# Kernel tuning notes

Hardware: AMD Instinct MI355X
Metric: run time of the kernel (lower is better)

## Reference

```python
import jax, jax.numpy as jnp
import numpy as np

B, N, C, H, NH, NC = 4, 2048, 256, 128, 8, 3  # batch, points, in_ch, hidden, heads, classes
DH = H // NH


def setup_inputs() -> dict:
    key = jax.random.key(0)
    ki = iter(jax.random.split(key, 48))
    def w(shape, s=0.05):
        return jax.random.normal(next(ki), shape, jnp.float32) * s
    z = lambda n: jnp.zeros((n,), jnp.float32)
    o = lambda n: jnp.ones((n,), jnp.float32)
    inp = dict(x=jax.random.normal(next(ki), (B, N, C), jnp.float32))
    inp.update(fuse_w1=w((H, C)), fuse_b1=z(H), fuse_w2=w((H, H)), fuse_b2=z(H))
    for l in range(2):
        inp[f'attn{l}_in_w'] = w((3 * H, H)); inp[f'attn{l}_in_b'] = z(3 * H)
        inp[f'attn{l}_out_w'] = w((H, H)); inp[f'attn{l}_out_b'] = z(H)
        inp[f'ffn{l}_w1'] = w((2 * H, H)); inp[f'ffn{l}_b1'] = z(2 * H)
        inp[f'ffn{l}_w2'] = w((H, 2 * H)); inp[f'ffn{l}_b2'] = z(H)
        inp[f'ln{2*l}_g'] = o(H); inp[f'ln{2*l}_b'] = z(H)
        inp[f'ln{2*l+1}_g'] = o(H); inp[f'ln{2*l+1}_b'] = z(H)
    inp.update(out_w1=w((H, H)), out_b1=z(H), out_w2=w((NC, H)), out_b2=z(NC))
    inp.update(det_w1=w((H // 2, H)), det_b1=z(H // 2), det_w2=w((1, H // 2)), det_b2=z(1))
    return inp


def _ln(x, g, b):
    m = jnp.mean(x, axis=-1, keepdims=True)
    v = jnp.mean((x - m) ** 2, axis=-1, keepdims=True)
    return (x - m) * jax.lax.rsqrt(v + 1e-5) * g + b


def _mha(x, in_w, in_b, out_w, out_b):
    # nn.MultiheadAttention (batch_first, self-attn), eval mode (no dropout)
    Bq, Nq, _ = x.shape
    qkv = x @ in_w.T + in_b                          # [B,N,3H]
    q, k, v = jnp.split(qkv, 3, axis=-1)
    q = q.reshape(Bq, Nq, NH, DH)
    k = k.reshape(Bq, Nq, NH, DH)
    v = v.reshape(Bq, Nq, NH, DH)
    s = jnp.einsum('bqhd,bkhd->bhqk', q, k) / jnp.sqrt(jnp.float32(DH))
    a = jax.nn.softmax(s, axis=-1)
    o = jnp.einsum('bhqk,bkhd->bqhd', a, v).reshape(Bq, Nq, H)
    return o @ out_w.T + out_b


def _forward(x, fuse_w1, fuse_b1, fuse_w2, fuse_b2,
             attn0_in_w, attn0_in_b, attn0_out_w, attn0_out_b,
             ffn0_w1, ffn0_b1, ffn0_w2, ffn0_b2, ln0_g, ln0_b, ln1_g, ln1_b,
             attn1_in_w, attn1_in_b, attn1_out_w, attn1_out_b,
             ffn1_w1, ffn1_b1, ffn1_w2, ffn1_b2, ln2_g, ln2_b, ln3_g, ln3_b,
             out_w1, out_b1, out_w2, out_b2, det_w1, det_b1, det_w2, det_b2):
    # feature_fusion (dropout = identity in eval)
    h = jnp.maximum(x @ fuse_w1.T + fuse_b1, 0) @ fuse_w2.T + fuse_b2
    layers = [
        (attn0_in_w, attn0_in_b, attn0_out_w, attn0_out_b, ffn0_w1, ffn0_b1, ffn0_w2, ffn0_b2, ln0_g, ln0_b, ln1_g, ln1_b),
        (attn1_in_w, attn1_in_b, attn1_out_w, attn1_out_b, ffn1_w1, ffn1_b1, ffn1_w2, ffn1_b2, ln2_g, ln2_b, ln3_g, ln3_b),
    ]
    for (iw, ib, ow, ob, f1w, f1b, f2w, f2b, g1, be1, g2, be2) in layers:
        h = _ln(h + _mha(h, iw, ib, ow, ob), g1, be1)
        h = _ln(h + (jnp.maximum(h @ f1w.T + f1b, 0) @ f2w.T + f2b), g2, be2)
    refined_logits = jnp.maximum(h @ out_w1.T + out_b1, 0) @ out_w2.T + out_b2   # [B,N,NC]
    head_prob = jax.nn.sigmoid(jnp.maximum(h @ det_w1.T + det_b1, 0) @ det_w2.T + det_b2)[..., 0]  # [B,N]
    quality = jnp.mean(head_prob, axis=1)                                        # [B]
    return refined_logits, head_prob, quality


def reference(x, fuse_w1, fuse_b1, fuse_w2, fuse_b2,
              attn0_in_w, attn0_in_b, attn0_out_w, attn0_out_b,
              ffn0_w1, ffn0_b1, ffn0_w2, ffn0_b2, ln0_g, ln0_b, ln1_g, ln1_b,
              attn1_in_w, attn1_in_b, attn1_out_w, attn1_out_b,
              ffn1_w1, ffn1_b1, ffn1_w2, ffn1_b2, ln2_g, ln2_b, ln3_g, ln3_b,
              out_w1, out_b1, out_w2, out_b2, det_w1, det_b1, det_w2, det_b2):
    return _forward(x, fuse_w1, fuse_b1, fuse_w2, fuse_b2,
                    attn0_in_w, attn0_in_b, attn0_out_w, attn0_out_b,
                    ffn0_w1, ffn0_b1, ffn0_w2, ffn0_b2, ln0_g, ln0_b, ln1_g, ln1_b,
                    attn1_in_w, attn1_in_b, attn1_out_w, attn1_out_b,
                    ffn1_w1, ffn1_b1, ffn1_w2, ffn1_b2, ln2_g, ln2_b, ln3_g, ln3_b,
                    out_w1, out_b1, out_w2, out_b2, det_w1, det_b1, det_w2, det_b2)
```

## Files before the change

kernel.cpp:

```cpp
#include <hip/hip_runtime.h>
#include <cstddef>

constexpr int Bb  = 4;
constexpr int Nn  = 2048;
constexpr int Cc  = 256;
constexpr int Hh  = 128;
constexpr int NHh = 8;
constexpr int DHh = 16;
constexpr int MTOK = Bb * Nn;
#define LOG2E 1.4426950408889634f

typedef __attribute__((ext_vector_type(8))) short bf16x8;
typedef __attribute__((ext_vector_type(4))) short bf16x4;
typedef __attribute__((ext_vector_type(4))) float f32x4;

__device__ __forceinline__ short f32_to_bf16_rne(float f) {
    union { float f; unsigned int u; } c; c.f = f;
    unsigned int r = c.u + 0x7fffu + ((c.u >> 16) & 1u);
    return (short)(r >> 16);
}
__device__ __forceinline__ float bf16_to_f32(short s) {
    union { float f; unsigned int u; } c; c.u = ((unsigned int)(unsigned short)s) << 16;
    return c.f;
}
__device__ __forceinline__ unsigned pack2_bf16(float a, float b) {
    unsigned r;
    asm("v_cvt_pk_bf16_f32 %0, %1, %2" : "=v"(r) : "v"(a), "v"(b));
    return r;
}

struct CvtJobs {
    const float* src[13];
    short*       dst[13];
    int          off[14];
    float*       qzero;
};

__global__ __launch_bounds__(256) void cvt_kernel(CvtJobs j) {
    const int gid = blockIdx.x * 256 + threadIdx.x;
    if (blockIdx.x == 0 && threadIdx.x < 4) j.qzero[threadIdx.x] = 0.f;
    if (gid >= j.off[13]) return;
    int k = 0;
    #pragma unroll
    for (int i = 0; i < 12; ++i) if (gid >= j.off[i + 1]) k = i + 1;
    const int idx = (gid - j.off[k]) * 4;
    float4 v = *(const float4*)(j.src[k] + idx);
    short o4[4] = { f32_to_bf16_rne(v.x), f32_to_bf16_rne(v.y),
                    f32_to_bf16_rne(v.z), f32_to_bf16_rne(v.w) };
    *(bf16x4*)(j.dst[k] + idx) = *(bf16x4*)o4;
}

__global__ __launch_bounds__(256) void qkv_gemm_kernel(
    const short* __restrict__ X, const short* __restrict__ W,
    const float* __restrict__ bias, short* __restrict__ Yb)
{
    constexpr int K = 128, N = 384, ST = K + 8;
    __shared__ short As[64 * ST];
    __shared__ short Bs[64 * ST];

    const int tid  = threadIdx.x;
    const int lane = tid & 63;
    const int wv   = tid >> 6;
    const int col  = lane & 15;
    const int g    = lane >> 4;
    const int m0   = blockIdx.y * 64;
    const int n0   = blockIdx.x * 64;

    for (int i = tid; i < 64 * (K / 8); i += 256) {
        const int r = i / (K / 8), c = (i % (K / 8)) * 8;
        *(bf16x8*)&As[r * ST + c] = *(const bf16x8*)(X + (size_t)(m0 + r) * K + c);
        *(bf16x8*)&Bs[r * ST + c] = *(const bf16x8*)(W + (size_t)(n0 + r) * K + c);
    }
    __syncthreads();

    f32x4 acc[4] = {};
    #pragma unroll
    for (int k0 = 0; k0 < K; k0 += 32) {
        bf16x8 a = *(bf16x8*)&As[(wv * 16 + col) * ST + k0 + g * 8];
        #pragma unroll
        for (int jj = 0; jj < 4; ++jj) {
            bf16x8 b = *(bf16x8*)&Bs[(jj * 16 + col) * ST + k0 + g * 8];
            acc[jj] = __builtin_amdgcn_mfma_f32_16x16x32_bf16(a, b, acc[jj], 0, 0, 0);
        }
    }

    #pragma unroll
    for (int jj = 0; jj < 4; ++jj) {
        const int cn = n0 + jj * 16 + col;
        const float bb = bias[cn];
        #pragma unroll
        for (int r = 0; r < 4; ++r) {
            const int rm = m0 + wv * 16 + g * 4 + r;
            Yb[(size_t)rm * N + cn] = f32_to_bf16_rne(acc[jj][r] + bb);
        }
    }
}

template<int K, int CR, bool DO_LN>
__global__ __launch_bounds__(256) void gemmln_kernel(
    const short* __restrict__ X, const short* __restrict__ W,
    const float* __restrict__ bias,
    float* __restrict__ hf, short* __restrict__ hb,
    const float* __restrict__ gw, const float* __restrict__ bw)
{
    constexpr int ST  = K + 8;
    constexpr int NCH = 128 / CR;
    constexpr int NF  = CR / 32;
    __shared__ short As[32 * ST];
    __shared__ short Ws[CR * ST];
    __shared__ float P[32 * 130];

    const int tid  = threadIdx.x;
    const int lane = tid & 63;
    const int wv   = tid >> 6;
    const int col  = lane & 15;
    const int g    = lane >> 4;
    const int m0   = blockIdx.x * 32;
    const int mst  = (wv & 1) * 16;
    const int cb   = (wv >> 1) * (CR / 2);

    for (int i = tid; i < 32 * (K / 8); i += 256) {
        const int r = i / (K / 8), c = (i % (K / 8)) * 8;
        *(bf16x8*)&As[r * ST + c] = *(const bf16x8*)(X + (size_t)(m0 + r) * K + c);
    }

    f32x4 ya[NCH][NF] = {};
    #pragma unroll
    for (int ch = 0; ch < NCH; ++ch) {
        for (int i = tid; i < CR * (K / 8); i += 256) {
            const int r = i / (K / 8), c = (i % (K / 8)) * 8;
            *(bf16x8*)&Ws[r * ST + c] =
                *(const bf16x8*)(W + (size_t)(ch * CR + r) * K + c);
        }
        __syncthreads();
        #pragma unroll
        for (int k0 = 0; k0 < K; k0 += 32) {
            bf16x8 a = *(bf16x8*)&As[(mst + col) * ST + k0 + g * 8];
            #pragma unroll
            for (int f = 0; f < NF; ++f) {
                bf16x8 b = *(bf16x8*)&Ws[(cb + f * 16 + col) * ST + k0 + g * 8];
                ya[ch][f] = __builtin_amdgcn_mfma_f32_16x16x32_bf16(a, b, ya[ch][f], 0, 0, 0);
            }
        }
        __syncthreads();
    }

    #pragma unroll
    for (int ch = 0; ch < NCH; ++ch)
        #pragma unroll
        for (int f = 0; f < NF; ++f) {
            const int cn = ch * CR + cb + f * 16 + col;
            const float bb = bias[cn];
            #pragma unroll
            for (int r = 0; r < 4; ++r)
                P[(mst + g * 4 + r) * 130 + cn] = ya[ch][f][r] + bb;
        }
    __syncthreads();

    #pragma unroll
    for (int rr = 0; rr < 8; ++rr) {
        const int row = wv * 8 + rr;
        const size_t t = m0 + row;
        float2 pv = *(float2*)&P[row * 130 + 2 * lane];
        if (DO_LN) {
            float2 hv = ((const float2*)(hf + t * Hh))[lane];
            float a0 = hv.x + pv.x, a1 = hv.y + pv.y;
            float sum = a0 + a1;
            #pragma unroll
            for (int off = 32; off > 0; off >>= 1) sum += __shfl_xor(sum, off);
            const float mean = sum * (1.f / 128.f);
            const float d0 = a0 - mean, d1 = a1 - mean;
            float vs = d0 * d0 + d1 * d1;
            #pragma unroll
            for (int off = 32; off > 0; off >>= 1) vs += __shfl_xor(vs, off);
            const float rstd = rsqrtf(vs * (1.f / 128.f) + 1e-5f);
            float2 gv = ((const float2*)gw)[lane];
            float2 bv = ((const float2*)bw)[lane];
            float2 r = { d0 * rstd * gv.x + bv.x, d1 * rstd * gv.y + bv.y };
            ((float2*)(hf + t * Hh))[lane] = r;
            *(unsigned*)&hb[t * Hh + lane * 2] = pack2_bf16(r.x, r.y);
        } else {
            ((float2*)(hf + t * Hh))[lane] = pv;
            *(unsigned*)&hb[t * Hh + lane * 2] = pack2_bf16(pv.x, pv.y);
        }
    }
}

template<int K, int MID, int CR1, int CR2, bool DO_LN>
__global__ __launch_bounds__(256) void mlp2_kernel(
    const short* __restrict__ X,
    const short* __restrict__ W1, const float* __restrict__ b1,
    const short* __restrict__ W2, const float* __restrict__ b2,
    float* __restrict__ hf, short* __restrict__ hb,
    const float* __restrict__ gw, const float* __restrict__ bw)
{
    constexpr int STA = K + 8;
    constexpr int STU = MID + 8;
    constexpr int WS1 = CR1 * STA;
    constexpr int WS2 = CR2 * STU;
    constexpr int WSZ = (WS1 > WS2) ? WS1 : WS2;
    __shared__ short As[32 * STA];
    __shared__ short Ws[WSZ];
    __shared__ short U[32 * STU];
    __shared__ float P[32 * 130];

    const int tid  = threadIdx.x;
    const int lane = tid & 63;
    const int wv   = tid >> 6;
    const int col  = lane & 15;
    const int g    = lane >> 4;
    const int m0   = blockIdx.x * 32;
    const int mst  = (wv & 1) * 16;

    for (int i = tid; i < 32 * (K / 8); i += 256) {
        const int r = i / (K / 8), c = (i % (K / 8)) * 8;
        *(bf16x8*)&As[r * STA + c] = *(const bf16x8*)(X + (size_t)(m0 + r) * K + c);
    }

    constexpr int NCH1 = MID / CR1;
    constexpr int NF1  = CR1 / 32;
    const int cb1 = (wv >> 1) * (CR1 / 2);
    #pragma unroll
    for (int ch = 0; ch < NCH1; ++ch) {
        for (int i = tid; i < CR1 * (K / 8); i += 256) {
            const int r = i / (K / 8), c = (i % (K / 8)) * 8;
            *(bf16x8*)&Ws[r * STA + c] =
                *(const bf16x8*)(W1 + (size_t)(ch * CR1 + r) * K + c);
        }
        __syncthreads();
        f32x4 ya[NF1] = {};
        #pragma unroll
        for (int k0 = 0; k0 < K; k0 += 32) {
            bf16x8 a = *(bf16x8*)&As[(mst + col) * STA + k0 + g * 8];
            #pragma unroll
            for (int f = 0; f < NF1; ++f) {
                bf16x8 b = *(bf16x8*)&Ws[(cb1 + f * 16 + col) * STA + k0 + g * 8];
                ya[f] = __builtin_amdgcn_mfma_f32_16x16x32_bf16(a, b, ya[f], 0, 0, 0);
            }
        }
        #pragma unroll
        for (int f = 0; f < NF1; ++f) {
            const int cn = ch * CR1 + cb1 + f * 16 + col;
            const float bb = b1[cn];
            #pragma unroll
            for (int r = 0; r < 4; ++r)
                U[(mst + g * 4 + r) * STU + cn] =
                    f32_to_bf16_rne(fmaxf(ya[f][r] + bb, 0.f));
        }
        __syncthreads();
    }

    constexpr int NCH2 = 128 / CR2;
    constexpr int NF2  = CR2 / 32;
    const int cb2 = (wv >> 1) * (CR2 / 2);
    f32x4 yb[NCH2][NF2] = {};
    #pragma unroll
    for (int ch = 0; ch < NCH2; ++ch) {
        for (int i = tid; i < CR2 * (MID / 8); i += 256) {
            const int r = i / (MID / 8), c = (i % (MID / 8)) * 8;
            *(bf16x8*)&Ws[r * STU + c] =
                *(const bf16x8*)(W2 + (size_t)(ch * CR2 + r) * MID + c);
        }
        __syncthreads();
        #pragma unroll
        for (int k0 = 0; k0 < MID; k0 += 32) {
            bf16x8 a = *(bf16x8*)&U[(mst + col) * STU + k0 + g * 8];
            #pragma unroll
            for (int f = 0; f < NF2; ++f) {
                bf16x8 b = *(bf16x8*)&Ws[(cb2 + f * 16 + col) * STU + k0 + g * 8];
                yb[ch][f] = __builtin_amdgcn_mfma_f32_16x16x32_bf16(a, b, yb[ch][f], 0, 0, 0);
            }
        }
        __syncthreads();
    }

    #pragma unroll
    for (int ch = 0; ch < NCH2; ++ch)
        #pragma unroll
        for (int f = 0; f < NF2; ++f) {
            const int cn = ch * CR2 + cb2 + f * 16 + col;
            const float bb = b2[cn];
            #pragma unroll
            for (int r = 0; r < 4; ++r)
                P[(mst + g * 4 + r) * 130 + cn] = yb[ch][f][r] + bb;
        }
    __syncthreads();

    #pragma unroll
    for (int rr = 0; rr < 8; ++rr) {
        const int row = wv * 8 + rr;
        const size_t t = m0 + row;
        float2 pv = *(float2*)&P[row * 130 + 2 * lane];
        if (DO_LN) {
            float2 hv = ((const float2*)(hf + t * Hh))[lane];
            float a0 = hv.x + pv.x, a1 = hv.y + pv.y;
            float sum = a0 + a1;
            #pragma unroll
            for (int off = 32; off > 0; off >>= 1) sum += __shfl_xor(sum, off);
            const float mean = sum * (1.f / 128.f);
            const float d0 = a0 - mean, d1 = a1 - mean;
            float vs = d0 * d0 + d1 * d1;
            #pragma unroll
            for (int off = 32; off > 0; off >>= 1) vs += __shfl_xor(vs, off);
            const float rstd = rsqrtf(vs * (1.f / 128.f) + 1e-5f);
            float2 gv = ((const float2*)gw)[lane];
            float2 bv = ((const float2*)bw)[lane];
            float2 r = { d0 * rstd * gv.x + bv.x, d1 * rstd * gv.y + bv.y };
            ((float2*)(hf + t * Hh))[lane] = r;
            *(unsigned*)&hb[t * Hh + lane * 2] = pack2_bf16(r.x, r.y);
        } else {
            ((float2*)(hf + t * Hh))[lane] = pv;
            *(unsigned*)&hb[t * Hh + lane * 2] = pack2_bf16(pv.x, pv.y);
        }
    }
}

__global__ __launch_bounds__(256) void head_kernel(
    const short* __restrict__ X,
    const short* __restrict__ W1b, const float* __restrict__ b1,
    const short* __restrict__ DW1b, const float* __restrict__ db1,
    const float* __restrict__ w2, const float* __restrict__ b2,
    const float* __restrict__ dw2, const float* __restrict__ db2,
    float* __restrict__ out)
{
    constexpr int K = 128, ST = K + 8;
    __shared__ short As[32 * ST];
    __shared__ short Ws[64 * ST];
    __shared__ float P[32 * 196];

    const int tid  = threadIdx.x;
    const int lane = tid & 63;
    const int wv   = tid >> 6;
    const int col  = lane & 15;
    const int g    = lane >> 4;
    const int m0   = blockIdx.x * 32;
    const int mst  = (wv & 1) * 16;
    const int cb   = (wv >> 1) * 32;

    for (int i = tid; i < 32 * (K / 8); i += 256) {
        const int r = i / (K / 8), c = (i % (K / 8)) * 8;
        *(bf16x8*)&As[r * ST + c] = *(const bf16x8*)(X + (size_t)(m0 + r) * K + c);
    }

    f32x4 ya[3][2] = {};
    #pragma unroll
    for (int ch = 0; ch < 3; ++ch) {
        for (int i = tid; i < 64 * (K / 8); i += 256) {
            const int r = i / (K / 8), c = (i % (K / 8)) * 8;
            const int rg = ch * 64 + r;
            const short* src = (rg < 128) ? (W1b + (size_t)rg * K)
                                          : (DW1b + (size_t)(rg - 128) * K);
            *(bf16x8*)&Ws[r * ST + c] = *(const bf16x8*)(src + c);
        }
        __syncthreads();
        #pragma unroll
        for (int k0 = 0; k0 < K; k0 += 32) {
            bf16x8 a = *(bf16x8*)&As[(mst + col) * ST + k0 + g * 8];
            #pragma unroll
            for (int f = 0; f < 2; ++f) {
                bf16x8 b = *(bf16x8*)&Ws[(cb + f * 16 + col) * ST + k0 + g * 8];
                ya[ch][f] = __builtin_amdgcn_mfma_f32_16x16x32_bf16(a, b, ya[ch][f], 0, 0, 0);
            }
        }
        __syncthreads();
    }

    #pragma unroll
    for (int ch = 0; ch < 3; ++ch)
        #pragma unroll
        for (int f = 0; f < 2; ++f) {
            const int cn = ch * 64 + cb + f * 16 + col;
            const float bb = (cn < 128) ? b1[cn] : db1[cn - 128];
            #pragma unroll
            for (int r = 0; r < 4; ++r)
                P[(mst + g * 4 + r) * 196 + cn] = fmaxf(ya[ch][f][r] + bb, 0.f);
        }
    __syncthreads();

    const float w20 = w2[2 * lane],       w21 = w2[2 * lane + 1];
    const float w22 = w2[128 + 2 * lane], w23 = w2[129 + 2 * lane];
    const float w24 = w2[256 + 2 * lane], w25 = w2[257 + 2 * lane];
    const float dwl = dw2[lane];
    float qacc = 0.f;
    #pragma unroll
    for (int rr = 0; rr < 8; ++rr) {
        const int row = wv * 8 + rr;
        const size_t t = m0 + row;
        const float x0 = P[row * 196 + 2 * lane];
        const float x1 = P[row * 196 + 2 * lane + 1];
        float s0 = x0 * w20 + x1 * w21;
        float s1 = x0 * w22 + x1 * w23;
        float s2 = x0 * w24 + x1 * w25;
        float d  = P[row * 196 + 128 + lane] * dwl;
        #pragma unroll
        for (int off = 32; off > 0; off >>= 1) {
            s0 += __shfl_xor(s0, off);
            s1 += __shfl_xor(s1, off);
            s2 += __shfl_xor(s2, off);
            d  += __shfl_xor(d,  off);
        }
        if (lane == 0) {
            out[t * 3 + 0] = s0 + b2[0];
            out[t * 3 + 1] = s1 + b2[1];
            out[t * 3 + 2] = s2 + b2[2];
            const float prob = 1.f / (1.f + __expf(-(d + db2[0])));
            out[24576 + t] = prob;
            qacc += prob;
        }
    }
    if (lane == 0)
        atomicAdd(&out[32768 + (m0 >> 11)], qacc * (1.f / (float)Nn));
}

constexpr int KT = 128;
constexpr int KS = 28;
constexpr int VS = 132;

__global__ __launch_bounds__(256) void attn_kernel(
    const short* __restrict__ qkv, short* __restrict__ out)
{
    __shared__ short Ks[KT * KS];
    __shared__ short Vs[DHh * VS];

    const int tid  = threadIdx.x;
    const int lane = tid & 63;
    const int wv   = tid >> 6;
    const int col  = lane & 15;
    const int g    = lane >> 4;
    const int hd   = blockIdx.y;
    const int b    = blockIdx.z;
    const int q0   = blockIdx.x * 64 + wv * 16;

    const short* base = qkv + (size_t)b * Nn * 384;

    bf16x8 qf = {};
    if (g < 2) {
        bf16x8 qraw = *(const bf16x8*)(base + (size_t)(q0 + col) * 384 + hd * DHh + g * 8);
        const float qs = 0.25f * LOG2E;
        #pragma unroll
        for (int i = 0; i < 8; ++i)
            qf[i] = f32_to_bf16_rne(bf16_to_f32(qraw[i]) * qs);
    }

    f32x4 o    = {0.f, 0.f, 0.f, 0.f};
    f32x4 lacc = {0.f, 0.f, 0.f, 0.f};
    const short one_bf16 = (short)0x3F80;
    const bf16x8 ones = { one_bf16, one_bf16, one_bf16, one_bf16,
                          one_bf16, one_bf16, one_bf16, one_bf16 };

    const int ksr = tid >> 1;
    const int ksd = (tid & 1) * 8;
    const int va  = tid >> 2;
    const int vd  = (tid & 3) * 4;

    const short* kptr = base + (size_t)ksr * 384 + Hh + hd * DHh + ksd;
    const short* vptr = base + (size_t)(2 * va) * 384 + 2 * Hh + hd * DHh + vd;
    bf16x8 kreg = *(const bf16x8*)kptr;
    bf16x4 vr0  = *(const bf16x4*)vptr;
    bf16x4 vr1  = *(const bf16x4*)(vptr + 384);

    for (int kt = 0; kt < Nn; kt += KT) {
        __syncthreads();

        *(bf16x8*)&Ks[ksr * KS + ksd] = kreg;
        {
            unsigned a0 = ((const unsigned*)&vr0)[0], a1 = ((const unsigned*)&vr0)[1];
            unsigned b0 = ((const unsigned*)&vr1)[0], b1 = ((const unsigned*)&vr1)[1];
            *(unsigned*)&Vs[(vd + 0) * VS + 2 * va] = __builtin_amdgcn_perm(b0, a0, 0x05040100);
            *(unsigned*)&Vs[(vd + 1) * VS + 2 * va] = __builtin_amdgcn_perm(b0, a0, 0x07060302);
            *(unsigned*)&Vs[(vd + 2) * VS + 2 * va] = __builtin_amdgcn_perm(b1, a1, 0x05040100);
            *(unsigned*)&Vs[(vd + 3) * VS + 2 * va] = __builtin_amdgcn_perm(b1, a1, 0x07060302);
        }

        if (kt + KT < Nn) {
            kptr += KT * 384;
            vptr += KT * 384;
            kreg = *(const bf16x8*)kptr;
            vr0  = *(const bf16x4*)vptr;
            vr1  = *(const bf16x4*)(vptr + 384);
        }

        asm volatile("s_waitcnt lgkmcnt(0)" ::: "memory");
        __builtin_amdgcn_s_barrier();

        __builtin_amdgcn_s_setprio(1);
        #pragma unroll
        for (int s = 0; s < 4; ++s) {
            bf16x8 kf0 = {}, kf1 = {};
            if (g < 2) {
                kf0 = *(bf16x8*)&Ks[(s * 32 + col) * KS + g * 8];
                kf1 = *(bf16x8*)&Ks[(s * 32 + 16 + col) * KS + g * 8];
            }
            f32x4 z = {0.f, 0.f, 0.f, 0.f};
            f32x4 sA = __builtin_amdgcn_mfma_f32_16x16x32_bf16(kf0, qf, z, 0, 0, 0);
            f32x4 sB = __builtin_amdgcn_mfma_f32_16x16x32_bf16(kf1, qf, z, 0, 0, 0);

            union { bf16x8 v; unsigned u[4]; } pf;
            pf.u[0] = pack2_bf16(__builtin_amdgcn_exp2f(sA[0]),
                                 __builtin_amdgcn_exp2f(sA[1]));
            pf.u[1] = pack2_bf16(__builtin_amdgcn_exp2f(sA[2]),
                                 __builtin_amdgcn_exp2f(sA[3]));
            pf.u[2] = pack2_bf16(__builtin_amdgcn_exp2f(sB[0]),
                                 __builtin_amdgcn_exp2f(sB[1]));
            pf.u[3] = pack2_bf16(__builtin_amdgcn_exp2f(sB[2]),
                                 __builtin_amdgcn_exp2f(sB[3]));

            bf16x8 vf;
            ((bf16x4*)&vf)[0] = *(bf16x4*)&Vs[col * VS + s * 32 + g * 4];
            ((bf16x4*)&vf)[1] = *(bf16x4*)&Vs[col * VS + s * 32 + 16 + g * 4];

            o    = __builtin_amdgcn_mfma_f32_16x16x32_bf16(pf.v, vf,   o,    0, 0, 0);
            lacc = __builtin_amdgcn_mfma_f32_16x16x32_bf16(pf.v, ones, lacc, 0, 0, 0);
        }
        __builtin_amdgcn_s_setprio(0);
    }

    #pragma unroll
    for (int r = 0; r < 4; ++r) {
        const float inv = __builtin_amdgcn_rcpf(lacc[r]);
        out[(size_t)(b * Nn + q0 + g * 4 + r) * Hh + hd * DHh + col] =
            f32_to_bf16_rne(o[r] * inv);
    }
}

extern "C" void kernel_launch(void* const* d_in, const int* in_sizes, int n_in,
                              void* d_out, int out_size, void* d_ws, size_t ws_size,
                              hipStream_t stream)
{
    char* W8 = (char*)d_ws;
    float* hf   = (float*)(W8 + 0);
    short* hb   = (short*)(W8 + 4194304);
    short* wb   = (short*)(W8 + 6291456);
    char*  regA = W8 + 7340032;
    char*  regB = W8 + 13631488;

    short* xb    = (short*)regA;
    short* qkvb  = (short*)regA;
    short* attno = (short*)regB;
    float* out   = (float*)d_out;

    const int wsz[12]  = {32768,16384,49152,16384,32768,32768,49152,16384,32768,32768,16384,8192};
    const int wsrc[12] = {1, 3, 5, 7, 9, 11, 17, 19, 21, 23, 29, 33};
    int woff[13]; woff[0] = 0;
    for (int i = 0; i < 12; ++i) woff[i + 1] = woff[i] + wsz[i];

    CvtJobs jobs;
    int acc = 0;
    for (int i = 0; i < 12; ++i) {
        jobs.src[i] = (const float*)d_in[wsrc[i]];
        jobs.dst[i] = wb + woff[i];
        jobs.off[i] = acc;
        acc += wsz[i] / 4;
    }
    jobs.src[12] = (const float*)d_in[0];
    jobs.dst[12] = xb;
    jobs.off[12] = acc;
    acc += (MTOK * Cc) / 4;
    jobs.off[13] = acc;
    jobs.qzero = out + 32768;

    hipLaunchKernelGGL(cvt_kernel, dim3((acc + 255) / 256), dim3(256), 0, stream, jobs);

    hipLaunchKernelGGL((mlp2_kernel<256, 128, 32, 64, false>), dim3(MTOK / 32), dim3(256), 0,
                       stream, xb, wb + woff[0], (const float*)d_in[2],
                       wb + woff[1], (const float*)d_in[4], hf, hb, nullptr, nullptr);

    for (int l = 0; l < 2; ++l) {
        const int ib = 5 + l * 12;
        const int wbase = 2 + l * 4;
        hipLaunchKernelGGL(qkv_gemm_kernel, dim3(384 / 64, MTOK / 64), dim3(256), 0, stream,
                           hb, wb + woff[wbase + 0], (const float*)d_in[ib + 1], qkvb);
        hipLaunchKernelGGL(attn_kernel, dim3(Nn / 64, NHh, Bb), dim3(256), 0, stream,
                           qkvb, attno);
        hipLaunchKernelGGL((gemmln_kernel<128, 64, true>), dim3(MTOK / 32), dim3(256), 0, stream,
                           attno, wb + woff[wbase + 1], (const float*)d_in[ib + 3],
                           hf, hb, (const float*)d_in[ib + 8], (const float*)d_in[ib + 9]);
        hipLaunchKernelGGL((mlp2_kernel<128, 256, 64, 32, true>), dim3(MTOK / 32), dim3(256), 0,
                           stream, hb, wb + woff[wbase + 2], (const float*)d_in[ib + 5],
                           wb + woff[wbase + 3], (const float*)d_in[ib + 7],
                           hf, hb, (const float*)d_in[ib + 10], (const float*)d_in[ib + 11]);
    }

    hipLaunchKernelGGL(head_kernel, dim3(MTOK / 32), dim3(256), 0, stream,
                       hb, wb + woff[10], (const float*)d_in[30],
                       wb + woff[11], (const float*)d_in[34],
                       (const float*)d_in[31], (const float*)d_in[32],
                       (const float*)d_in[35], (const float*)d_in[36], out);
}
```

Baseline: 289.0 us.

## Shrink row tile to 16 tokens and alias LDS epilogue buffer onto weight tile

The fused GEMM+LayerNorm and two-layer MLP kernels now process 16 token rows per block instead of 32, doubling the grid. Each wave owns one 16-column slice per 64-row weight chunk, and K is split into 128-wide stages so the weight tile stays a fixed 64x136. The fp32 epilogue buffer P now reuses the weight-tile shared memory rather than having its own allocation. The aim is lower LDS and register use per block, giving more resident blocks and better latency hiding. The cost is that each weight matrix is reloaded from global/L2 twice as many times in total.

```diff
diff --git a/kernel.cpp b/kernel.cpp
--- a/kernel.cpp
+++ b/kernel.cpp
@@ -96,70 +96,62 @@
     }
 }
 
-template<int K, int CR, bool DO_LN>
+template<int K, bool DO_LN>
 __global__ __launch_bounds__(256) void gemmln_kernel(
     const short* __restrict__ X, const short* __restrict__ W,
     const float* __restrict__ bias,
     float* __restrict__ hf, short* __restrict__ hb,
     const float* __restrict__ gw, const float* __restrict__ bw)
 {
-    constexpr int ST  = K + 8;
-    constexpr int NCH = 128 / CR;
-    constexpr int NF  = CR / 32;
-    __shared__ short As[32 * ST];
-    __shared__ short Ws[CR * ST];
-    __shared__ float P[32 * 130];
+    constexpr int ST = K + 8;
+    __shared__ short As[16 * ST];
+    __shared__ short Ws[64 * 136];
+    float* P = (float*)Ws;
 
     const int tid  = threadIdx.x;
     const int lane = tid & 63;
     const int wv   = tid >> 6;
     const int col  = lane & 15;
     const int g    = lane >> 4;
-    const int m0   = blockIdx.x * 32;
-    const int mst  = (wv & 1) * 16;
-    const int cb   = (wv >> 1) * (CR / 2);
-
-    for (int i = tid; i < 32 * (K / 8); i += 256) {
+    const int m0   = blockIdx.x * 16;
+    const int cb   = wv * 16;
+
+    for (int i = tid; i < 16 * (K / 8); i += 256) {
         const int r = i / (K / 8), c = (i % (K / 8)) * 8;
         *(bf16x8*)&As[r * ST + c] = *(const bf16x8*)(X + (size_t)(m0 + r) * K + c);
     }
 
-    f32x4 ya[NCH][NF] = {};
-    #pragma unroll
-    for (int ch = 0; ch < NCH; ++ch) {
-        for (int i = tid; i < CR * (K / 8); i += 256) {
+    f32x4 ya[2] = {};
+    #pragma unroll
+    for (int ch = 0; ch < 2; ++ch) {
+        for (int i = tid; i < 64 * (K / 8); i += 256) {
             const int r = i / (K / 8), c = (i % (K / 8)) * 8;
-            *(bf16x8*)&Ws[r * ST + c] =
-                *(const bf16x8*)(W + (size_t)(ch * CR + r) * K + c);
+            *(bf16x8*)&Ws[r * 136 + c] =
+                *(const bf16x8*)(W + (size_t)(ch * 64 + r) * K + c);
         }
         __syncthreads();
         #pragma unroll
         for (int k0 = 0; k0 < K; k0 += 32) {
-            bf16x8 a = *(bf16x8*)&As[(mst + col) * ST + k0 + g * 8];
-            #pragma unroll
-            for (int f = 0; f < NF; ++f) {
-                bf16x8 b = *(bf16x8*)&Ws[(cb + f * 16 + col) * ST + k0 + g * 8];
-                ya[ch][f] = __builtin_amdgcn_mfma_f32_16x16x32_bf16(a, b, ya[ch][f], 0, 0, 0);
-            }
+            bf16x8 a = *(bf16x8*)&As[col * ST + k0 + g * 8];
+            bf16x8 b = *(bf16x8*)&Ws[(cb + col) * 136 + k0 + g * 8];
+            ya[ch] = __builtin_amdgcn_mfma_f32_16x16x32_bf16(a, b, ya[ch], 0, 0, 0);
         }
         __syncthreads();
     }
 
     #pragma unroll
-    for (int ch = 0; ch < NCH; ++ch)
-        #pragma unroll
-        for (int f = 0; f < NF; ++f) {
-            const int cn = ch * CR + cb + f * 16 + col;
-            const float bb = bias[cn];
-            #pragma unroll
-            for (int r = 0; r < 4; ++r)
-                P[(mst + g * 4 + r) * 130 + cn] = ya[ch][f][r] + bb;
-        }
+    for (int ch = 0; ch < 2; ++ch) {
+        const int cn = ch * 64 + cb + col;
+        const float bb = bias[cn];
+        #pragma unroll
+        for (int r = 0; r < 4; ++r)
+            P[(g * 4 + r) * 130 + cn] = ya[ch][r] + bb;
+    }
     __syncthreads();
 
     #pragma unroll
-    for (int rr = 0; rr < 8; ++rr) {
-        const int row = wv * 8 + rr;
+    for (int rr = 0; rr < 4; ++rr) {
+        const int row = wv * 4 + rr;
         const size_t t = m0 + row;
         float2 pv = *(float2*)&P[row * 130 + 2 * lane];
         if (DO_LN) {
@@ -186,7 +178,7 @@
     }
 }
 
-template<int K, int MID, int CR1, int CR2, bool DO_LN>
+template<int K, int MID, bool DO_LN>
 __global__ __launch_bounds__(256) void mlp2_kernel(
     const short* __restrict__ X,
     const short* __restrict__ W1, const float* __restrict__ b1,
@@ -196,99 +188,87 @@
 {
     constexpr int STA = K + 8;
     constexpr int STU = MID + 8;
-    constexpr int WS1 = CR1 * STA;
-    constexpr int WS2 = CR2 * STU;
-    constexpr int WSZ = (WS1 > WS2) ? WS1 : WS2;
-    __shared__ short As[32 * STA];
-    __shared__ short Ws[WSZ];
-    __shared__ short U[32 * STU];
-    __shared__ float P[32 * 130];
+    __shared__ short As[16 * STA];
+    __shared__ short Ws[64 * 136];
+    __shared__ short U[16 * STU];
+    float* P = (float*)Ws;
 
     const int tid  = threadIdx.x;
     const int lane = tid & 63;
     const int wv   = tid >> 6;
     const int col  = lane & 15;
     const int g    = lane >> 4;
-    const int m0   = blockIdx.x * 32;
-    const int mst  = (wv & 1) * 16;
-
-    for (int i = tid; i < 32 * (K / 8); i += 256) {
+    const int m0   = blockIdx.x * 16;
+    const int cb   = wv * 16;
+
+    for (int i = tid; i < 16 * (K / 8); i += 256) {
         const int r = i / (K / 8), c = (i % (K / 8)) * 8;
         *(bf16x8*)&As[r * STA + c] = *(const bf16x8*)(X + (size_t)(m0 + r) * K + c);
     }
 
-    constexpr int NCH1 = MID / CR1;
-    constexpr int NF1  = CR1 / 32;
-    const int cb1 = (wv >> 1) * (CR1 / 2);
+    constexpr int KP1  = K / 128;
+    constexpr int NCH1 = MID / 64;
     #pragma unroll
     for (int ch = 0; ch < NCH1; ++ch) {
-        for (int i = tid; i < CR1 * (K / 8); i += 256) {
-            const int r = i / (K / 8), c = (i % (K / 8)) * 8;
-            *(bf16x8*)&Ws[r * STA + c] =
-                *(const bf16x8*)(W1 + (size_t)(ch * CR1 + r) * K + c);
-        }
-        __syncthreads();
-        f32x4 ya[NF1] = {};
-        #pragma unroll
-        for (int k0 = 0; k0 < K; k0 += 32) {
-            bf16x8 a = *(bf16x8*)&As[(mst + col) * STA + k0 + g * 8];
-            #pragma unroll
-            for (int f = 0; f < NF1; ++f) {
-                bf16x8 b = *(bf16x8*)&Ws[(cb1 + f * 16 + col) * STA + k0 + g * 8];
-                ya[f] = __builtin_amdgcn_mfma_f32_16x16x32_bf16(a, b, ya[f], 0, 0, 0);
+        f32x4 ya = {};
+        #pragma unroll
+        for (int kh = 0; kh < KP1; ++kh) {
+            for (int i = tid; i < 64 * 16; i += 256) {
+                const int r = i / 16, c = (i % 16) * 8;
+                *(bf16x8*)&Ws[r * 136 + c] =
+                    *(const bf16x8*)(W1 + (size_t)(ch * 64 + r) * K + kh * 128 + c);
             }
-        }
-        #pragma unroll
-        for (int f = 0; f < NF1; ++f) {
-            const int cn = ch * CR1 + cb1 + f * 16 + col;
-            const float bb = b1[cn];
-            #pragma unroll
-            for (int r = 0; r < 4; ++r)
-                U[(mst + g * 4 + r) * STU + cn] =
-                    f32_to_bf16_rne(fmaxf(ya[f][r] + bb, 0.f));
-        }
-        __syncthreads();
-    }
-
-    constexpr int NCH2 = 128 / CR2;
-    constexpr int NF2  = CR2 / 32;
-    const int cb2 = (wv >> 1) * (CR2 / 2);
-    f32x4 yb[NCH2][NF2] = {};
-    #pragma unroll
-    for (int ch = 0; ch < NCH2; ++ch) {
-        for (int i = tid; i < CR2 * (MID / 8); i += 256) {
-            const int r = i / (MID / 8), c = (i % (MID / 8)) * 8;
-            *(bf16x8*)&Ws[r * STU + c] =
-                *(const bf16x8*)(W2 + (size_t)(ch * CR2 + r) * MID + c);
-        }
-        __syncthreads();
-        #pragma unroll
-        for (int k0 = 0; k0 < MID; k0 += 32) {
-            bf16x8 a = *(bf16x8*)&U[(mst + col) * STU + k0 + g * 8];
-            #pragma unroll
-            for (int f = 0; f < NF2; ++f) {
-                bf16x8 b = *(bf16x8*)&Ws[(cb2 + f * 16 + col) * STU + k0 + g * 8];
-                yb[ch][f] = __builtin_amdgcn_mfma_f32_16x16x32_bf16(a, b, yb[ch][f], 0, 0, 0);
+            __syncthreads();
+            #pragma unroll
+            for (int k0 = 0; k0 < 128; k0 += 32) {
+                bf16x8 a = *(bf16x8*)&As[col * STA + kh * 128 + k0 + g * 8];
+                bf16x8 b = *(bf16x8*)&Ws[(cb + col) * 136 + k0 + g * 8];
+                ya = __builtin_amdgcn_mfma_f32_16x16x32_bf16(a, b, ya, 0, 0, 0);
             }
-        }
-        __syncthreads();
-    }
-
-    #pragma unroll
-    for (int ch = 0; ch < NCH2; ++ch)
-        #pragma unroll
-        for (int f = 0; f < NF2; ++f) {
-            const int cn = ch * CR2 + cb2 + f * 16 + col;
-            const float bb = b2[cn];
-            #pragma unroll
-            for (int r = 0; r < 4; ++r)
-                P[(mst + g * 4 + r) * 130 + cn] = yb[ch][f][r] + bb;
-        }
+            __syncthreads();
+        }
+        const int cn = ch * 64 + cb + col;
+        const float bb = b1[cn];
+        #pragma unroll
+        for (int r = 0; r < 4; ++r)
+            U[(g * 4 + r) * STU + cn] = f32_to_bf16_rne(fmaxf(ya[r] + bb, 0.f));
+    }
+
+    constexpr int KP2 = MID / 128;
+    f32x4 yb[2] = {};
+    #pragma unroll
+    for (int ch2 = 0; ch2 < 2; ++ch2) {
+        #pragma unroll
+        for (int kh = 0; kh < KP2; ++kh) {
+            for (int i = tid; i < 64 * 16; i += 256) {
+                const int r = i / 16, c = (i % 16) * 8;
+                *(bf16x8*)&Ws[r * 136 + c] =
+                    *(const bf16x8*)(W2 + (size_t)(ch2 * 64 + r) * MID + kh * 128 + c);
+            }
+            __syncthreads();
+            #pragma unroll
+            for (int k0 = 0; k0 < 128; k0 += 32) {
+                bf16x8 a = *(bf16x8*)&U[col * STU + kh * 128 + k0 + g * 8];
+                bf16x8 b = *(bf16x8*)&Ws[(cb + col) * 136 + k0 + g * 8];
+                yb[ch2] = __builtin_amdgcn_mfma_f32_16x16x32_bf16(a, b, yb[ch2], 0, 0, 0);
+            }
+            __syncthreads();
+        }
+    }
+
+    #pragma unroll
+    for (int ch2 = 0; ch2 < 2; ++ch2) {
+        const int cn = ch2 * 64 + cb + col;
+        const float bb = b2[cn];
+        #pragma unroll
+        for (int r = 0; r < 4; ++r)
+            P[(g * 4 + r) * 130 + cn] = yb[ch2][r] + bb;
+    }
     __syncthreads();
 
     #pragma unroll
-    for (int rr = 0; rr < 8; ++rr) {
-        const int row = wv * 8 + rr;
+    for (int rr = 0; rr < 4; ++rr) {
+        const int row = wv * 4 + rr;
         const size_t t = m0 + row;
         float2 pv = *(float2*)&P[row * 130 + 2 * lane];
         if (DO_LN) {
@@ -561,7 +541,7 @@
 
     hipLaunchKernelGGL(cvt_kernel, dim3((acc + 255) / 256), dim3(256), 0, stream, jobs);
 
-    hipLaunchKernelGGL((mlp2_kernel<256, 128, 32, 64, false>), dim3(MTOK / 32), dim3(256), 0,
+    hipLaunchKernelGGL((mlp2_kernel<256, 128, false>), dim3(MTOK / 16), dim3(256), 0,
                        stream, xb, wb + woff[0], (const float*)d_in[2],
                        wb + woff[1], (const float*)d_in[4], hf, hb, nullptr, nullptr);
 
@@ -572,10 +552,10 @@
                            hb, wb + woff[wbase + 0], (const float*)d_in[ib + 1], qkvb);
         hipLaunchKernelGGL(attn_kernel, dim3(Nn / 64, NHh, Bb), dim3(256), 0, stream,
                            qkvb, attno);
-        hipLaunchKernelGGL((gemmln_kernel<128, 64, true>), dim3(MTOK / 32), dim3(256), 0, stream,
+        hipLaunchKernelGGL((gemmln_kernel<128, true>), dim3(MTOK / 16), dim3(256), 0, stream,
                            attno, wb + woff[wbase + 1], (const float*)d_in[ib + 3],
                            hf, hb, (const float*)d_in[ib + 8], (const float*)d_in[ib + 9]);
-        hipLaunchKernelGGL((mlp2_kernel<128, 256, 64, 32, true>), dim3(MTOK / 32), dim3(256), 0,
+        hipLaunchKernelGGL((mlp2_kernel<128, 256, true>), dim3(MTOK / 16), dim3(256), 0,
                            stream, hb, wb + woff[wbase + 2], (const float*)d_in[ib + 5],
                            wb + woff[wbase + 3], (const float*)d_in[ib + 7],
                            hf, hb, (const float*)d_in[ib + 10], (const float*)d_in[ib + 11]);
```

Measured after the change: 285.6 us. No clear change (-1.2%).
